# Performance work log

Hardware: AMD Instinct MI355X
Metric: run time of the kernel (lower is better)

The kernel has to match this reference:

```python
import jax, jax.numpy as jnp
import numpy as np

H = 256   # node_hidden_dim == edge_hidden_dim

def _ln(x, g, b):
    m = x.mean(-1, keepdims=True)
    v = ((x - m) ** 2).mean(-1, keepdims=True)
    return (x - m) / jnp.sqrt(v + 1e-5) * g + b

def _slnn(x, W, b, g, beta):
    # Linear -> LayerNorm -> ReLU (SingleLayerNN)
    return jax.nn.relu(_ln(x @ W.T + b, g, beta))

def _gru_mean(x, Wih, Whh, bih, bhh):
    # x: [E, T, Din]; torch GRU gate order (r, z, n); returns mean over time of outputs [E, H]
    h0 = jnp.zeros((x.shape[0], Whh.shape[1]), x.dtype)
    def step(h, xt):
        gi = xt @ Wih.T + bih
        gh = h @ Whh.T + bhh
        ir, iz, inn = jnp.split(gi, 3, axis=-1)
        hr, hz, hn = jnp.split(gh, 3, axis=-1)
        r = jax.nn.sigmoid(ir + hr)
        z = jax.nn.sigmoid(iz + hz)
        n = jnp.tanh(inn + r * hn)
        h_new = (1.0 - z) * n + z * h
        return h_new, h_new
    _, ys = jax.lax.scan(step, h0, jnp.swapaxes(x, 0, 1))  # [T, E, H]
    return ys.mean(axis=0)

def setup_inputs() -> dict:
    key = jax.random.key(0)
    ks = iter(jax.random.split(key, 64))
    rn = lambda shape, s=1.0: (jax.random.normal(next(ks), shape, jnp.float32) * s)
    ru = lambda shape: jax.random.uniform(next(ks), shape, jnp.float32)
    ri = lambda shape, hi: jax.random.randint(next(ks), shape, 0, hi, jnp.int32)
    N0, N1, N2, E0, E1, T = 40000, 10000, 2000, 100000, 20000, 8
    Dn, De, FC, C = 128, 64, 512, 16
    inp = {
        'node_features': rn((N0, Dn)),
        'edge_features_0': rn((E0, T, De)),
        'edge_features_1': rn((E1, T, H)),
        'history_0': rn((N0, H)),
        'history_1': rn((N1, H)),
        'agg_history_1': rn((N2, H)),
        'subg_norm_1': ru((N1, 1)),
        'subg_norm_2': ru((N2, 1)),
        'norm_2': ru((N2, 1)),
        'src0': ri((E0,), N0), 'dst0': ri((E0,), N1),
        'src1': ri((E1,), N1), 'dst1': ri((E1,), N2),
        'self_nid0': ri((N1,), N0), 'self_nid1': ri((N2,), N1),
        # parameters
        'gru0_Wih': rn((3 * H, De), 0.05), 'gru0_Whh': rn((3 * H, H), 0.05),
        'gru0_bih': rn((3 * H,), 0.05), 'gru0_bhh': rn((3 * H,), 0.05),
        'gru1_Wih': rn((3 * H, H), 0.05), 'gru1_Whh': rn((3 * H, H), 0.05),
        'gru1_bih': rn((3 * H,), 0.05), 'gru1_bhh': rn((3 * H,), 0.05),
        'phi0_W': rn((H, Dn + H), 0.05), 'phi0_b': rn((H,), 0.05),
        'phi0_g': jnp.ones((H,)), 'phi0_beta': jnp.zeros((H,)),
        'phi1_W': rn((H, 2 * H), 0.05), 'phi1_b': rn((H,), 0.05),
        'phi1_g': jnp.ones((H,)), 'phi1_beta': jnp.zeros((H,)),
        'nu0_W': rn((H, 2 * H), 0.05), 'nu0_b': rn((H,), 0.05),
        'nu0_g': jnp.ones((H,)), 'nu0_beta': jnp.zeros((H,)),
        'nu1_W': rn((H, 2 * H), 0.05), 'nu1_b': rn((H,), 0.05),
        'nu1_g': jnp.ones((H,)), 'nu1_beta': jnp.zeros((H,)),
        'fc1_W': rn((FC, H), 0.05), 'fc1_b': rn((FC,), 0.05),
        'fc2_W': rn((C, FC), 0.05), 'fc2_b': rn((C,), 0.05),
    }
    return inp

def reference(node_features, edge_features_0, edge_features_1, history_0, history_1,
              agg_history_1, subg_norm_1, subg_norm_2, norm_2,
              gru0_Wih, gru0_Whh, gru0_bih, gru0_bhh,
              gru1_Wih, gru1_Whh, gru1_bih, gru1_bhh,
              phi0_W, phi0_b, phi0_g, phi0_beta,
              phi1_W, phi1_b, phi1_g, phi1_beta,
              nu0_W, nu0_b, nu0_g, nu0_beta,
              nu1_W, nu1_b, nu1_g, nu1_beta,
              fc1_W, fc1_b, fc2_W, fc2_b,
              src0, dst0, src1, dst1, self_nid0, self_nid1):
    N1, N2 = self_nid0.shape[0], self_nid1.shape[0]
    # ---- layer 0 ----
    self_h0 = _slnn(jnp.concatenate([jnp.zeros((N1, H), node_features.dtype),
                                     node_features[self_nid0]], 1),
                    phi0_W, phi0_b, phi0_g, phi0_beta)                       # [N1, H]
    edge_emb0 = _gru_mean(edge_features_0, gru0_Wih, gru0_Whh, gru0_bih, gru0_bhh)  # [E0, H]
    nb0 = _slnn(jnp.concatenate([node_features[src0], edge_emb0], 1),
                phi0_W, phi0_b, phi0_g, phi0_beta)
    msg0 = jax.nn.relu(nb0 - history_0[src0])
    delta_nb0 = jax.ops.segment_sum(msg0, dst0, num_segments=N1)             # scatter-sum
    new_h0 = (delta_nb0 - self_h0) * subg_norm_1
    h1 = _slnn(jnp.concatenate([new_h0, self_h0], 1), nu0_W, nu0_b, nu0_g, nu0_beta)  # [N1, H]
    # ---- layer 1 ----
    self_h1 = _slnn(jnp.concatenate([jnp.zeros((N2, H), h1.dtype), h1[self_nid1]], 1),
                    phi1_W, phi1_b, phi1_g, phi1_beta)                       # [N2, H]
    self_delta_h1 = self_h1 - history_1[self_nid1]
    edge_emb1 = _gru_mean(edge_features_1, gru1_Wih, gru1_Whh, gru1_bih, gru1_bhh)  # [E1, H]
    nb1 = _slnn(jnp.concatenate([h1[src1], edge_emb1], 1),
                phi1_W, phi1_b, phi1_g, phi1_beta)
    msg1 = jax.nn.relu(nb1 - history_1[src1])
    delta_nb1 = jax.ops.segment_sum(msg1, dst1, num_segments=N2)
    new_h1 = (delta_nb1 - self_delta_h1) * subg_norm_2 + agg_history_1 * norm_2
    h2 = _slnn(jnp.concatenate([new_h1, self_h1], 1), nu1_W, nu1_b, nu1_g, nu1_beta)  # [N2, H]
    # ---- readout (no activation between fc1 and fc2, as in source) ----
    logit = (h2 @ fc1_W.T + fc1_b) @ fc2_W.T + fc2_b
    return logit
```

## Files before the change

### kernel.cpp

```cpp
#include <hip/hip_runtime.h>

typedef unsigned short u16;
typedef __attribute__((ext_vector_type(4))) float f32x4;
typedef __attribute__((ext_vector_type(8))) short bf16x8;
#define MFMA16(a,b,c) __builtin_amdgcn_mfma_f32_16x16x32_bf16((a),(b),(c),0,0,0)

__device__ __forceinline__ u16 f2bf(float f){
  unsigned int u = __float_as_uint(f);
  u += 0x7FFFu + ((u >> 16) & 1u);
  return (u16)(u >> 16);
}
__device__ __forceinline__ float bf2f(u16 h){
  return __uint_as_float(((unsigned int)h) << 16);
}
__device__ __forceinline__ float sigmoid_f(float x){
  x = fminf(fmaxf(x, -30.f), 30.f);
  return __fdividef(1.f, 1.f + __expf(-x));
}
__device__ __forceinline__ float tanh_f(float x){
  x = fminf(fmaxf(x, -15.f), 15.f);
  float e = __expf(-2.f * x);
  return __fdividef(1.f - e, 1.f + e);
}

__global__ void cvt_bf16_kernel(const float* __restrict__ in, u16* __restrict__ out, int n){
  int i = blockIdx.x * 256 + threadIdx.x;
  int stride = gridDim.x * 256;
  for (; i < n; i += stride) out[i] = f2bf(in[i]);
}

template<int R>
__device__ __forceinline__ void ln_stats_rows(const float* __restrict__ O,
                                              float* __restrict__ mean_s,
                                              float* __restrict__ rstd_s){
  const int tid  = threadIdx.x;
  const int wave = tid >> 6, lane = tid & 63;
  constexpr int RW = R / 4;
  #pragma unroll
  for (int rr = 0; rr < RW; rr++){
    const int r = wave * RW + rr;
    float s = 0.f, q = 0.f;
    #pragma unroll
    for (int i = lane; i < 256; i += 64){ float v = O[r*256 + i]; s += v; q += v*v; }
    #pragma unroll
    for (int off = 32; off; off >>= 1){ s += __shfl_down(s, off); q += __shfl_down(q, off); }
    if (lane == 0){
      float m   = s * (1.f/256.f);
      float var = q * (1.f/256.f) - m*m;
      mean_s[r] = m;
      rstd_s[r] = rsqrtf(fmaxf(var, 0.f) + 1e-5f);
    }
  }
}

template<int DIN, int NFD>
__global__ __launch_bounds__(256, 2)
void gru_mfma_kernel(int E,
    const float* __restrict__ x,
    const float* __restrict__ nodef,
    const int*   __restrict__ src,
    const int*   __restrict__ dst,
    const float* __restrict__ hist,
    const u16*   __restrict__ Wih,
    const u16*   __restrict__ Whh,
    const float* __restrict__ bih,
    const float* __restrict__ bhh,
    const u16*   __restrict__ phiW,
    const float* __restrict__ phib,
    const float* __restrict__ phig,
    const float* __restrict__ phibeta,
    float* __restrict__ delta)
{
  constexpr int HP  = 264;
  constexpr int XW  = (DIN > NFD) ? DIN : NFD;
  constexpr int XLP = XW + 8;
  constexpr int KP  = NFD + 256;

  __shared__ u16  hb[2 * 32 * HP];
  __shared__ u16  xl[32 * XLP];
  __shared__ float sums_s[4 * 32], sqs_s[4 * 32];
  __shared__ float mean_s[32], rstd_s[32];
  __shared__ int   srcs_s[32], dsts_s[32];

  const int tid  = threadIdx.x;
  const int wave = tid >> 6, lane = tid & 63;
  const int quad = lane >> 4, ln15 = lane & 15;
  const int cbase = wave * 64;
  const int e0   = blockIdx.x * 32;

  if (tid < 32){
    int e = e0 + tid;
    int ec = (e < E) ? e : (E - 1);
    srcs_s[tid] = src[ec];
    dsts_s[tid] = dst[ec];
  }

  int cnt[4];
  float brc[4], bzc[4], bnic[4], bnhc[4], pb[4], gg[4], gb[4];
  #pragma unroll
  for (int nt = 0; nt < 4; nt++){
    int c = cbase + nt*16 + ln15;
    cnt[nt]  = c;
    brc[nt]  = bih[c]       + bhh[c];
    bzc[nt]  = bih[256 + c] + bhh[256 + c];
    bnic[nt] = bih[512 + c];
    bnhc[nt] = bhh[512 + c];
    pb[nt]   = phib[c];
    gg[nt]   = phig[c];
    gb[nt]   = phibeta[c];
  }

  const int aoff = ln15 * HP  + quad * 8;
  const int xoff = ln15 * XLP + quad * 8;
  const int qoff = quad * 8;

  float hs[2][4][4];
  #pragma unroll
  for (int mt = 0; mt < 2; mt++)
    #pragma unroll
    for (int nt = 0; nt < 4; nt++)
      #pragma unroll
      for (int q = 0; q < 4; q++) hs[mt][nt][q] = 0.f;

  const f32x4 zero4 = {0.f, 0.f, 0.f, 0.f};

  for (int t = 0; t < 8; t++){
    __syncthreads();
    {
      constexpr int R4 = DIN / 4;
      for (int i = tid; i < 32 * R4; i += 256){
        int e  = i / R4;
        int k4 = (i - e * R4) * 4;
        int ge = (e0 + e < E) ? (e0 + e) : (E - 1);
        const float4 v = *(const float4*)(x + (size_t)ge * (8 * DIN) + (size_t)t * DIN + k4);
        ushort4 u;
        u.x = f2bf(v.x); u.y = f2bf(v.y); u.z = f2bf(v.z); u.w = f2bf(v.w);
        *(ushort4*)(xl + e * XLP + k4) = u;
      }
    }
    __syncthreads();

    const u16* rd = hb + ((t & 1) ^ 1) * (32 * HP);
    u16*       wr = hb + (t & 1) * (32 * HP);

    #pragma unroll 1
    for (int half = 0; half < 2; half++){
      f32x4 aR[2][2], aZ[2][2], aNI[2][2], aNH[2][2];
      #pragma unroll
      for (int mt = 0; mt < 2; mt++)
        #pragma unroll
        for (int j = 0; j < 2; j++){
          aR[mt][j] = zero4; aZ[mt][j] = zero4; aNI[mt][j] = zero4; aNH[mt][j] = zero4;
        }

      if (t > 0){
        #pragma unroll
        for (int kt = 0; kt < 8; kt++){
          bf16x8 a0 = *(const bf16x8*)(rd + aoff + kt * 32);
          bf16x8 a1 = *(const bf16x8*)(rd + aoff + 16 * HP + kt * 32);
          #pragma unroll
          for (int j = 0; j < 2; j++){
            const int nt = half * 2 + j;
            const u16* bp = Whh + (size_t)cnt[nt] * 256 + kt * 32 + qoff;
            bf16x8 br = *(const bf16x8*)(bp);
            bf16x8 bz = *(const bf16x8*)(bp + 256 * 256);
            bf16x8 bn = *(const bf16x8*)(bp + 512 * 256);
            aR[0][j]  = MFMA16(a0, br, aR[0][j]);  aR[1][j]  = MFMA16(a1, br, aR[1][j]);
            aZ[0][j]  = MFMA16(a0, bz, aZ[0][j]);  aZ[1][j]  = MFMA16(a1, bz, aZ[1][j]);
            aNH[0][j] = MFMA16(a0, bn, aNH[0][j]); aNH[1][j] = MFMA16(a1, bn, aNH[1][j]);
          }
        }
      }
      #pragma unroll
      for (int kt = 0; kt < DIN / 32; kt++){
        bf16x8 a0 = *(const bf16x8*)(xl + xoff + kt * 32);
        bf16x8 a1 = *(const bf16x8*)(xl + xoff + 16 * XLP + kt * 32);
        #pragma unroll
        for (int j = 0; j < 2; j++){
          const int nt = half * 2 + j;
          const u16* bp = Wih + (size_t)cnt[nt] * DIN + kt * 32 + qoff;
          bf16x8 br = *(const bf16x8*)(bp);
          bf16x8 bz = *(const bf16x8*)(bp + 256 * DIN);
          bf16x8 bn = *(const bf16x8*)(bp + 512 * DIN);
          aR[0][j]  = MFMA16(a0, br, aR[0][j]);  aR[1][j]  = MFMA16(a1, br, aR[1][j]);
          aZ[0][j]  = MFMA16(a0, bz, aZ[0][j]);  aZ[1][j]  = MFMA16(a1, bz, aZ[1][j]);
          aNI[0][j] = MFMA16(a0, bn, aNI[0][j]); aNI[1][j] = MFMA16(a1, bn, aNI[1][j]);
        }
      }
      #pragma unroll
      for (int mt = 0; mt < 2; mt++)
        #pragma unroll
        for (int j = 0; j < 2; j++){
          const int nt = half * 2 + j;
          const int c  = cnt[nt];
          #pragma unroll
          for (int q = 0; q < 4; q++){
            const int e = mt * 16 + quad * 4 + q;
            float r = sigmoid_f(aR[mt][j][q] + brc[nt]);
            float z = sigmoid_f(aZ[mt][j][q] + bzc[nt]);
            float n = tanh_f(aNI[mt][j][q] + bnic[nt] + r * (aNH[mt][j][q] + bnhc[nt]));
            float hold = (t > 0) ? bf2f(rd[e * HP + c]) : 0.f;
            float hnew = (1.f - z) * n + z * hold;
            hs[mt][nt][q] += hnew;
            if (t < 7) wr[e * HP + c] = f2bf(hnew);
          }
        }
    }
  }

  __syncthreads();
  {
    u16* eb = hb;
    #pragma unroll
    for (int mt = 0; mt < 2; mt++)
      #pragma unroll
      for (int nt = 0; nt < 4; nt++)
        #pragma unroll
        for (int q = 0; q < 4; q++){
          const int e = mt * 16 + quad * 4 + q;
          eb[e * HP + cnt[nt]] = f2bf(hs[mt][nt][q] * 0.125f);
        }
    constexpr int R4 = NFD / 4;
    for (int i = tid; i < 32 * R4; i += 256){
      int e  = i / R4;
      int k4 = (i - e * R4) * 4;
      const float4 v = *(const float4*)(nodef + (size_t)srcs_s[e] * NFD + k4);
      ushort4 u;
      u.x = f2bf(v.x); u.y = f2bf(v.y); u.z = f2bf(v.z); u.w = f2bf(v.w);
      *(ushort4*)(xl + e * XLP + k4) = u;
    }
  }
  __syncthreads();

  f32x4 P[2][4];
  #pragma unroll
  for (int mt = 0; mt < 2; mt++)
    #pragma unroll
    for (int nt = 0; nt < 4; nt++) P[mt][nt] = zero4;

  #pragma unroll
  for (int kt = 0; kt < NFD / 32; kt++){
    bf16x8 a0 = *(const bf16x8*)(xl + xoff + kt * 32);
    bf16x8 a1 = *(const bf16x8*)(xl + xoff + 16 * XLP + kt * 32);
    #pragma unroll
    for (int nt = 0; nt < 4; nt++){
      const u16* bp = phiW + (size_t)cnt[nt] * KP + kt * 32 + qoff;
      bf16x8 b = *(const bf16x8*)(bp);
      P[0][nt] = MFMA16(a0, b, P[0][nt]);
      P[1][nt] = MFMA16(a1, b, P[1][nt]);
    }
  }
  #pragma unroll
  for (int kt = 0; kt < 8; kt++){
    bf16x8 a0 = *(const bf16x8*)(hb + aoff + kt * 32);
    bf16x8 a1 = *(const bf16x8*)(hb + aoff + 16 * HP + kt * 32);
    #pragma unroll
    for (int nt = 0; nt < 4; nt++){
      const u16* bp = phiW + (size_t)cnt[nt] * KP + NFD + kt * 32 + qoff;
      bf16x8 b = *(const bf16x8*)(bp);
      P[0][nt] = MFMA16(a0, b, P[0][nt]);
      P[1][nt] = MFMA16(a1, b, P[1][nt]);
    }
  }

  float sl[2][4], sq[2][4];
  #pragma unroll
  for (int mt = 0; mt < 2; mt++)
    #pragma unroll
    for (int q = 0; q < 4; q++){ sl[mt][q] = 0.f; sq[mt][q] = 0.f; }
  #pragma unroll
  for (int mt = 0; mt < 2; mt++)
    #pragma unroll
    for (int nt = 0; nt < 4; nt++)
      #pragma unroll
      for (int q = 0; q < 4; q++){
        float v = P[mt][nt][q] + pb[nt];
        P[mt][nt][q] = v;
        sl[mt][q] += v;
        sq[mt][q] += v * v;
      }
  #pragma unroll
  for (int off = 1; off < 16; off <<= 1){
    #pragma unroll
    for (int mt = 0; mt < 2; mt++)
      #pragma unroll
      for (int q = 0; q < 4; q++){
        sl[mt][q] += __shfl_xor(sl[mt][q], off);
        sq[mt][q] += __shfl_xor(sq[mt][q], off);
      }
  }
  if (ln15 == 0){
    #pragma unroll
    for (int mt = 0; mt < 2; mt++)
      #pragma unroll
      for (int q = 0; q < 4; q++){
        int row = mt * 16 + quad * 4 + q;
        sums_s[wave * 32 + row] = sl[mt][q];
        sqs_s[wave * 32 + row]  = sq[mt][q];
      }
  }
  __syncthreads();
  if (tid < 32){
    float m = 0.f, qq = 0.f;
    #pragma unroll
    for (int w = 0; w < 4; w++){ m += sums_s[w * 32 + tid]; qq += sqs_s[w * 32 + tid]; }
    m  *= (1.f / 256.f);
    qq *= (1.f / 256.f);
    mean_s[tid] = m;
    rstd_s[tid] = rsqrtf(fmaxf(qq - m * m, 0.f) + 1e-5f);
  }
  __syncthreads();

  #pragma unroll
  for (int mt = 0; mt < 2; mt++)
    #pragma unroll
    for (int nt = 0; nt < 4; nt++){
      const int c = cnt[nt];
      #pragma unroll
      for (int q = 0; q < 4; q++){
        const int e  = mt * 16 + quad * 4 + q;
        const int ge = e0 + e;
        float y = (P[mt][nt][q] - mean_s[e]) * rstd_s[e] * gg[nt] + gb[nt];
        y = fmaxf(y, 0.f);
        float mv = y - hist[(size_t)srcs_s[e] * 256 + c];
        if (ge < E && mv > 0.f)
          atomicAdd(delta + (size_t)dsts_s[e] * 256 + c, mv);
      }
    }
}

template<int K, int WS>
__global__ __launch_bounds__(256)
void self_slnn_kernel(int N,
    const float* __restrict__ feat,
    const int*   __restrict__ nid,
    const float* __restrict__ W,
    const float* __restrict__ b,
    const float* __restrict__ g,
    const float* __restrict__ beta,
    const float* __restrict__ hist,
    float* __restrict__ out,
    float* __restrict__ out2)
{
  constexpr int R = 8;
  __shared__ float X[R*K];
  __shared__ float O[R*256];
  __shared__ float mean_s[R], rstd_s[R];
  __shared__ int   nids[R];
  const int tid = threadIdx.x;
  const int n0  = blockIdx.x * R;
  if (tid < R) nids[tid] = (n0 + tid < N) ? nid[n0 + tid] : 0;
  __syncthreads();
  for (int i = tid; i < R*K; i += 256){
    int r = i / K, k = i - r*K;
    X[i] = feat[(size_t)nids[r]*K + k];
  }
  __syncthreads();
  const int c = tid;
  const float* Wc = W + (size_t)c*WS + (WS - K);
  float acc[R];
  const float bc0 = b[c];
  #pragma unroll
  for (int r = 0; r < R; r++) acc[r] = bc0;
  #pragma unroll 1
  for (int k = 0; k < K; k += 4){
    float4 w = *(const float4*)(Wc + k);
    #pragma unroll
    for (int r = 0; r < R; r++){
      float4 xv = *(const float4*)(X + r*K + k);
      acc[r] += w.x*xv.x + w.y*xv.y + w.z*xv.z + w.w*xv.w;
    }
  }
  #pragma unroll
  for (int r = 0; r < R; r++) O[r*256 + c] = acc[r];
  __syncthreads();
  ln_stats_rows<R>(O, mean_s, rstd_s);
  __syncthreads();
  const float gc = g[c], bc = beta[c];
  #pragma unroll
  for (int r = 0; r < R; r++){
    int n = n0 + r;
    if (n < N){
      float y = fmaxf((acc[r] - mean_s[r]) * rstd_s[r] * gc + bc, 0.f);
      out[(size_t)n*256 + c] = y;
      if (out2) out2[(size_t)n*256 + c] = y - hist[(size_t)nids[r]*256 + c];
    }
  }
}

__global__ __launch_bounds__(256)
void compose_slnn_kernel(int N,
    const float* __restrict__ delta,
    const float* __restrict__ selfA,
    const float* __restrict__ selfB,
    const float* __restrict__ subg,
    const float* __restrict__ agg,
    const float* __restrict__ normv,
    const float* __restrict__ W,
    const float* __restrict__ b,
    const float* __restrict__ g,
    const float* __restrict__ beta,
    float* __restrict__ out)
{
  constexpr int R = 8;
  __shared__ float X[R*512];
  __shared__ float O[R*256];
  __shared__ float mean_s[R], rstd_s[R];
  const int tid = threadIdx.x;
  const int n0  = blockIdx.x * R;
  for (int i = tid; i < R*512; i += 256){
    int r = i >> 9, k = i & 511;
    int n = n0 + r;
    float v = 0.f;
    if (n < N){
      if (k < 256){
        v = (delta[(size_t)n*256 + k] - selfA[(size_t)n*256 + k]) * subg[n];
        if (agg) v += agg[(size_t)n*256 + k] * normv[n];
      } else {
        v = selfB[(size_t)n*256 + (k - 256)];
      }
    }
    X[i] = v;
  }
  __syncthreads();
  const int c = tid;
  const float* Wc = W + (size_t)c*512;
  float acc[R];
  const float bc0 = b[c];
  #pragma unroll
  for (int r = 0; r < R; r++) acc[r] = bc0;
  #pragma unroll 1
  for (int k = 0; k < 512; k += 4){
    float4 w = *(const float4*)(Wc + k);
    #pragma unroll
    for (int r = 0; r < R; r++){
      float4 xv = *(const float4*)(X + r*512 + k);
      acc[r] += w.x*xv.x + w.y*xv.y + w.z*xv.z + w.w*xv.w;
    }
  }
  #pragma unroll
  for (int r = 0; r < R; r++) O[r*256 + c] = acc[r];
  __syncthreads();
  ln_stats_rows<R>(O, mean_s, rstd_s);
  __syncthreads();
  const float gc = g[c], bc = beta[c];
  #pragma unroll
  for (int r = 0; r < R; r++){
    int n = n0 + r;
    if (n < N)
      out[(size_t)n*256 + c] = fmaxf((acc[r] - mean_s[r]) * rstd_s[r] * gc + bc, 0.f);
  }
}

__global__ __launch_bounds__(256)
void readout_kernel(int N,
    const float* __restrict__ h2,
    const float* __restrict__ W1,
    const float* __restrict__ b1,
    const float* __restrict__ W2,
    const float* __restrict__ b2,
    float* __restrict__ out)
{
  constexpr int R = 8;
  __shared__ float X[R*256];
  __shared__ float T[R*512];
  const int tid = threadIdx.x;
  const int n0  = blockIdx.x * R;
  for (int i = tid; i < R*256; i += 256){
    int r = i >> 8, k = i & 255;
    int n = n0 + r;
    X[i] = (n < N) ? h2[(size_t)n*256 + k] : 0.f;
  }
  __syncthreads();
  const int c = tid;
  const float* Wa = W1 + (size_t)c*256;
  const float* Wb = W1 + (size_t)(c+256)*256;
  float acca[R], accb[R];
  const float ba = b1[c], bb = b1[c+256];
  #pragma unroll
  for (int r = 0; r < R; r++){ acca[r] = ba; accb[r] = bb; }
  #pragma unroll 1
  for (int k = 0; k < 256; k += 4){
    float4 wa = *(const float4*)(Wa + k);
    float4 wb = *(const float4*)(Wb + k);
    #pragma unroll
    for (int r = 0; r < R; r++){
      float4 xv = *(const float4*)(X + r*256 + k);
      acca[r] += wa.x*xv.x + wa.y*xv.y + wa.z*xv.z + wa.w*xv.w;
      accb[r] += wb.x*xv.x + wb.y*xv.y + wb.z*xv.z + wb.w*xv.w;
    }
  }
  #pragma unroll
  for (int r = 0; r < R; r++){ T[r*512 + c] = acca[r]; T[r*512 + 256 + c] = accb[r]; }
  __syncthreads();
  if (tid < R*16){
    int r = tid >> 4, o = tid & 15;
    int n = n0 + r;
    if (n < N){
      float s = b2[o];
      const float* w  = W2 + (size_t)o*512;
      const float* tr = T + r*512;
      #pragma unroll 4
      for (int k = 0; k < 512; k++) s += tr[k]*w[k];
      out[(size_t)n*16 + o] = s;
    }
  }
}

extern "C" void kernel_launch(void* const* d_in, const int* in_sizes, int n_in,
                              void* d_out, int out_size, void* d_ws, size_t ws_size,
                              hipStream_t stream) {
  const float* nf     = (const float*)d_in[0];
  const float* x0     = (const float*)d_in[1];
  const float* x1     = (const float*)d_in[2];
  const float* hist0  = (const float*)d_in[3];
  const float* hist1  = (const float*)d_in[4];
  const float* aggh1  = (const float*)d_in[5];
  const float* subg1  = (const float*)d_in[6];
  const float* subg2  = (const float*)d_in[7];
  const float* norm2  = (const float*)d_in[8];
  const int*   src0   = (const int*)d_in[9];
  const int*   dst0   = (const int*)d_in[10];
  const int*   src1   = (const int*)d_in[11];
  const int*   dst1   = (const int*)d_in[12];
  const int*   nid0   = (const int*)d_in[13];
  const int*   nid1   = (const int*)d_in[14];
  const float* g0Wih  = (const float*)d_in[15];
  const float* g0Whh  = (const float*)d_in[16];
  const float* g0bih  = (const float*)d_in[17];
  const float* g0bhh  = (const float*)d_in[18];
  const float* g1Wih  = (const float*)d_in[19];
  const float* g1Whh  = (const float*)d_in[20];
  const float* g1bih  = (const float*)d_in[21];
  const float* g1bhh  = (const float*)d_in[22];
  const float* phi0W  = (const float*)d_in[23];
  const float* phi0b  = (const float*)d_in[24];
  const float* phi0g  = (const float*)d_in[25];
  const float* phi0be = (const float*)d_in[26];
  const float* phi1W  = (const float*)d_in[27];
  const float* phi1b  = (const float*)d_in[28];
  const float* phi1g  = (const float*)d_in[29];
  const float* phi1be = (const float*)d_in[30];
  const float* nu0W   = (const float*)d_in[31];
  const float* nu0b   = (const float*)d_in[32];
  const float* nu0g   = (const float*)d_in[33];
  const float* nu0be  = (const float*)d_in[34];
  const float* nu1W   = (const float*)d_in[35];
  const float* nu1b   = (const float*)d_in[36];
  const float* nu1g   = (const float*)d_in[37];
  const float* nu1be  = (const float*)d_in[38];
  const float* fc1W   = (const float*)d_in[39];
  const float* fc1b   = (const float*)d_in[40];
  const float* fc2W   = (const float*)d_in[41];
  const float* fc2b   = (const float*)d_in[42];

  const int E0 = in_sizes[9];
  const int E1 = in_sizes[11];
  const int N1 = in_sizes[13];
  const int N2 = in_sizes[14];

  float* ws     = (float*)d_ws;
  float* delta0 = ws;
  float* selfh0 = delta0 + (size_t)N1*256;
  float* h1p    = selfh0 + (size_t)N1*256;
  float* delta1 = h1p    + (size_t)N1*256;
  float* selfh1 = delta1 + (size_t)N2*256;
  float* selfd1 = selfh1 + (size_t)N2*256;
  float* h2p    = selfd1 + (size_t)N2*256;

  u16* wbf       = (u16*)(h2p + (size_t)N2*256);
  u16* g0Wih_bf  = wbf;
  u16* g0Whh_bf  = g0Wih_bf + 768*64;
  u16* phi0W_bf  = g0Whh_bf + 768*256;
  u16* g1Wih_bf  = phi0W_bf + 256*384;
  u16* g1Whh_bf  = g1Wih_bf + 768*256;
  u16* phi1W_bf  = g1Whh_bf + 768*256;

  hipMemsetAsync(delta0, 0, (size_t)N1*256*sizeof(float), stream);
  hipMemsetAsync(delta1, 0, (size_t)N2*256*sizeof(float), stream);

  cvt_bf16_kernel<<<192, 256, 0, stream>>>(g0Wih, g0Wih_bf, 768*64);
  cvt_bf16_kernel<<<768, 256, 0, stream>>>(g0Whh, g0Whh_bf, 768*256);
  cvt_bf16_kernel<<<384, 256, 0, stream>>>(phi0W, phi0W_bf, 256*384);
  cvt_bf16_kernel<<<768, 256, 0, stream>>>(g1Wih, g1Wih_bf, 768*256);
  cvt_bf16_kernel<<<768, 256, 0, stream>>>(g1Whh, g1Whh_bf, 768*256);
  cvt_bf16_kernel<<<512, 256, 0, stream>>>(phi1W, phi1W_bf, 256*512);

  const int gN1 = (N1 + 7) / 8;
  const int gN2 = (N2 + 7) / 8;

  self_slnn_kernel<128, 384><<<gN1, 256, 0, stream>>>(
      N1, nf, nid0, phi0W, phi0b, phi0g, phi0be, nullptr, selfh0, nullptr);

  gru_mfma_kernel<64, 128><<<(E0 + 31) / 32, 256, 0, stream>>>(
      E0, x0, nf, src0, dst0, hist0,
      g0Wih_bf, g0Whh_bf, g0bih, g0bhh,
      phi0W_bf, phi0b, phi0g, phi0be, delta0);

  compose_slnn_kernel<<<gN1, 256, 0, stream>>>(
      N1, delta0, selfh0, selfh0, subg1, nullptr, nullptr,
      nu0W, nu0b, nu0g, nu0be, h1p);

  self_slnn_kernel<256, 512><<<gN2, 256, 0, stream>>>(
      N2, h1p, nid1, phi1W, phi1b, phi1g, phi1be, hist1, selfh1, selfd1);

  gru_mfma_kernel<256, 256><<<(E1 + 31) / 32, 256, 0, stream>>>(
      E1, x1, h1p, src1, dst1, hist1,
      g1Wih_bf, g1Whh_bf, g1bih, g1bhh,
      phi1W_bf, phi1b, phi1g, phi1be, delta1);

  compose_slnn_kernel<<<gN2, 256, 0, stream>>>(
      N2, delta1, selfd1, selfh1, subg2, aggh1, norm2,
      nu1W, nu1b, nu1g, nu1be, h2p);

  readout_kernel<<<gN2, 256, 0, stream>>>(
      N2, h2p, fc1W, fc1b, fc2W, fc2b, (float*)d_out);

  (void)n_in; (void)out_size; (void)ws_size;
}
```

Before: 3.261 ms.

## Retile GRU kernel to 64-edge blocks with weight reuse and prefetched inputs

```diff
diff --git a/kernel.cpp b/kernel.cpp
--- a/kernel.cpp
+++ b/kernel.cpp
@@ -4,6 +4,8 @@
 typedef __attribute__((ext_vector_type(4))) float f32x4;
 typedef __attribute__((ext_vector_type(8))) short bf16x8;
 #define MFMA16(a,b,c) __builtin_amdgcn_mfma_f32_16x16x32_bf16((a),(b),(c),0,0,0)
+
+template<int N> struct ic { static constexpr int v = N; };
 
 __device__ __forceinline__ u16 f2bf(float f){
   unsigned int u = __float_as_uint(f);
@@ -54,7 +56,7 @@
 }
 
 template<int DIN, int NFD>
-__global__ __launch_bounds__(256, 2)
+__global__ __launch_bounds__(512, 2)
 void gru_mfma_kernel(int E,
     const float* __restrict__ x,
     const float* __restrict__ nodef,
@@ -72,35 +74,35 @@
     float* __restrict__ delta)
 {
   constexpr int HP  = 264;
-  constexpr int XW  = (DIN > NFD) ? DIN : NFD;
-  constexpr int XLP = XW + 8;
+  constexpr int XP  = DIN + 8;
+  constexpr int NP  = NFD + 8;
   constexpr int KP  = NFD + 256;
-
-  __shared__ u16  hb[2 * 32 * HP];
-  __shared__ u16  xl[32 * XLP];
-  __shared__ float sums_s[4 * 32], sqs_s[4 * 32];
-  __shared__ float mean_s[32], rstd_s[32];
-  __shared__ int   srcs_s[32], dsts_s[32];
+  constexpr int NF4 = DIN / 32;
+
+  __shared__ u16  hb[2 * 64 * HP];
+  __shared__ u16  xb[2 * 64 * XP];
+  __shared__ float sums_s[8 * 64], sqs_s[8 * 64];
+  __shared__ float mean_s[64], rstd_s[64];
+  __shared__ int   srcs_s[64], dsts_s[64];
 
   const int tid  = threadIdx.x;
   const int wave = tid >> 6, lane = tid & 63;
   const int quad = lane >> 4, ln15 = lane & 15;
-  const int cbase = wave * 64;
-  const int e0   = blockIdx.x * 32;
-
-  if (tid < 32){
-    int e = e0 + tid;
+  const int cbase = wave * 32;
+  const int e0   = blockIdx.x * 64;
+
+  if (tid < 64){
+    int e  = e0 + tid;
     int ec = (e < E) ? e : (E - 1);
     srcs_s[tid] = src[ec];
     dsts_s[tid] = dst[ec];
   }
 
-  int cnt[4];
-  float brc[4], bzc[4], bnic[4], bnhc[4], pb[4], gg[4], gb[4];
-  #pragma unroll
-  for (int nt = 0; nt < 4; nt++){
-    int c = cbase + nt*16 + ln15;
-    cnt[nt]  = c;
+  int cn[2]; float brc[2], bzc[2], bnic[2], bnhc[2], pb[2], gg[2], gb[2];
+  #pragma unroll
+  for (int nt = 0; nt < 2; nt++){
+    int c   = cbase + nt * 16 + ln15;
+    cn[nt]  = c;
     brc[nt]  = bih[c]       + bhh[c];
     bzc[nt]  = bih[256 + c] + bhh[256 + c];
     bnic[nt] = bih[512 + c];
@@ -110,200 +112,219 @@
     gb[nt]   = phibeta[c];
   }
 
-  const int aoff = ln15 * HP  + quad * 8;
-  const int xoff = ln15 * XLP + quad * 8;
-  const int qoff = quad * 8;
+  #pragma unroll
+  for (int j = 0; j < NF4; j++){
+    int i4 = tid + j * 512;
+    int e  = i4 / (DIN / 4);
+    int k4 = (i4 % (DIN / 4)) * 4;
+    int ge = (e0 + e < E) ? (e0 + e) : (E - 1);
+    float4 v = *(const float4*)(x + (size_t)ge * (8 * DIN) + k4);
+    ushort4 u;
+    u.x = f2bf(v.x); u.y = f2bf(v.y); u.z = f2bf(v.z); u.w = f2bf(v.w);
+    *(ushort4*)(xb + e * XP + k4) = u;
+  }
+  __syncthreads();
 
   float hs[2][4][4];
   #pragma unroll
-  for (int mt = 0; mt < 2; mt++)
-    #pragma unroll
-    for (int nt = 0; nt < 4; nt++)
-      #pragma unroll
-      for (int q = 0; q < 4; q++) hs[mt][nt][q] = 0.f;
+  for (int nt = 0; nt < 2; nt++)
+    #pragma unroll
+    for (int mt = 0; mt < 4; mt++)
+      #pragma unroll
+      for (int q = 0; q < 4; q++) hs[nt][mt][q] = 0.f;
 
   const f32x4 zero4 = {0.f, 0.f, 0.f, 0.f};
 
+  #pragma unroll 1
   for (int t = 0; t < 8; t++){
-    __syncthreads();
-    {
-      constexpr int R4 = DIN / 4;
-      for (int i = tid; i < 32 * R4; i += 256){
-        int e  = i / R4;
-        int k4 = (i - e * R4) * 4;
+    const u16* rd = hb + ((t & 1) ^ 1) * (64 * HP);
+    u16*       wr = hb + (t & 1) * (64 * HP);
+    const u16* xr = xb + (t & 1) * (64 * XP);
+
+    float4 xpre[NF4];
+    if (t < 7){
+      #pragma unroll
+      for (int j = 0; j < NF4; j++){
+        int i4 = tid + j * 512;
+        int e  = i4 / (DIN / 4);
+        int k4 = (i4 % (DIN / 4)) * 4;
         int ge = (e0 + e < E) ? (e0 + e) : (E - 1);
-        const float4 v = *(const float4*)(x + (size_t)ge * (8 * DIN) + (size_t)t * DIN + k4);
-        ushort4 u;
-        u.x = f2bf(v.x); u.y = f2bf(v.y); u.z = f2bf(v.z); u.w = f2bf(v.w);
-        *(ushort4*)(xl + e * XLP + k4) = u;
-      }
-    }
-    __syncthreads();
-
-    const u16* rd = hb + ((t & 1) ^ 1) * (32 * HP);
-    u16*       wr = hb + (t & 1) * (32 * HP);
-
-    #pragma unroll 1
-    for (int half = 0; half < 2; half++){
-      f32x4 aR[2][2], aZ[2][2], aNI[2][2], aNH[2][2];
-      #pragma unroll
-      for (int mt = 0; mt < 2; mt++)
-        #pragma unroll
-        for (int j = 0; j < 2; j++){
-          aR[mt][j] = zero4; aZ[mt][j] = zero4; aNI[mt][j] = zero4; aNH[mt][j] = zero4;
-        }
-
+        xpre[j] = *(const float4*)(x + (size_t)ge * (8 * DIN) + (size_t)(t + 1) * DIN + k4);
+      }
+    }
+
+    auto phase = [&](auto ntc){
+      constexpr int NT = decltype(ntc)::v;
+      const int c = cn[NT];
+      f32x4 aR[4], aZ[4], aNI[4], aNH[4];
+      #pragma unroll
+      for (int mt = 0; mt < 4; mt++){
+        aR[mt] = zero4; aZ[mt] = zero4; aNI[mt] = zero4; aNH[mt] = zero4;
+      }
       if (t > 0){
         #pragma unroll
         for (int kt = 0; kt < 8; kt++){
-          bf16x8 a0 = *(const bf16x8*)(rd + aoff + kt * 32);
-          bf16x8 a1 = *(const bf16x8*)(rd + aoff + 16 * HP + kt * 32);
+          bf16x8 a[4];
           #pragma unroll
-          for (int j = 0; j < 2; j++){
-            const int nt = half * 2 + j;
-            const u16* bp = Whh + (size_t)cnt[nt] * 256 + kt * 32 + qoff;
-            bf16x8 br = *(const bf16x8*)(bp);
-            bf16x8 bz = *(const bf16x8*)(bp + 256 * 256);
-            bf16x8 bn = *(const bf16x8*)(bp + 512 * 256);
-            aR[0][j]  = MFMA16(a0, br, aR[0][j]);  aR[1][j]  = MFMA16(a1, br, aR[1][j]);
-            aZ[0][j]  = MFMA16(a0, bz, aZ[0][j]);  aZ[1][j]  = MFMA16(a1, bz, aZ[1][j]);
-            aNH[0][j] = MFMA16(a0, bn, aNH[0][j]); aNH[1][j] = MFMA16(a1, bn, aNH[1][j]);
+          for (int mt = 0; mt < 4; mt++)
+            a[mt] = *(const bf16x8*)(rd + (mt*16 + ln15) * HP + kt * 32 + quad * 8);
+          const u16* bp = Whh + (size_t)c * 256 + kt * 32 + quad * 8;
+          bf16x8 br = *(const bf16x8*)(bp);
+          bf16x8 bz = *(const bf16x8*)(bp + 256 * 256);
+          bf16x8 bn = *(const bf16x8*)(bp + 512 * 256);
+          #pragma unroll
+          for (int mt = 0; mt < 4; mt++){
+            aR[mt]  = MFMA16(a[mt], br, aR[mt]);
+            aZ[mt]  = MFMA16(a[mt], bz, aZ[mt]);
+            aNH[mt] = MFMA16(a[mt], bn, aNH[mt]);
           }
         }
       }
       #pragma unroll
       for (int kt = 0; kt < DIN / 32; kt++){
-        bf16x8 a0 = *(const bf16x8*)(xl + xoff + kt * 32);
-        bf16x8 a1 = *(const bf16x8*)(xl + xoff + 16 * XLP + kt * 32);
+        bf16x8 a[4];
         #pragma unroll
-        for (int j = 0; j < 2; j++){
-          const int nt = half * 2 + j;
-          const u16* bp = Wih + (size_t)cnt[nt] * DIN + kt * 32 + qoff;
-          bf16x8 br = *(const bf16x8*)(bp);
-          bf16x8 bz = *(const bf16x8*)(bp + 256 * DIN);
-          bf16x8 bn = *(const bf16x8*)(bp + 512 * DIN);
-          aR[0][j]  = MFMA16(a0, br, aR[0][j]);  aR[1][j]  = MFMA16(a1, br, aR[1][j]);
-          aZ[0][j]  = MFMA16(a0, bz, aZ[0][j]);  aZ[1][j]  = MFMA16(a1, bz, aZ[1][j]);
-          aNI[0][j] = MFMA16(a0, bn, aNI[0][j]); aNI[1][j] = MFMA16(a1, bn, aNI[1][j]);
+        for (int mt = 0; mt < 4; mt++)
+          a[mt] = *(const bf16x8*)(xr + (mt*16 + ln15) * XP + kt * 32 + quad * 8);
+        const u16* bp = Wih + (size_t)c * DIN + kt * 32 + quad * 8;
+        bf16x8 br = *(const bf16x8*)(bp);
+        bf16x8 bz = *(const bf16x8*)(bp + 256 * DIN);
+        bf16x8 bn = *(const bf16x8*)(bp + 512 * DIN);
+        #pragma unroll
+        for (int mt = 0; mt < 4; mt++){
+          aR[mt]  = MFMA16(a[mt], br, aR[mt]);
+          aZ[mt]  = MFMA16(a[mt], bz, aZ[mt]);
+          aNI[mt] = MFMA16(a[mt], bn, aNI[mt]);
         }
       }
       #pragma unroll
-      for (int mt = 0; mt < 2; mt++)
-        #pragma unroll
-        for (int j = 0; j < 2; j++){
-          const int nt = half * 2 + j;
-          const int c  = cnt[nt];
-          #pragma unroll
-          for (int q = 0; q < 4; q++){
-            const int e = mt * 16 + quad * 4 + q;
-            float r = sigmoid_f(aR[mt][j][q] + brc[nt]);
-            float z = sigmoid_f(aZ[mt][j][q] + bzc[nt]);
-            float n = tanh_f(aNI[mt][j][q] + bnic[nt] + r * (aNH[mt][j][q] + bnhc[nt]));
-            float hold = (t > 0) ? bf2f(rd[e * HP + c]) : 0.f;
-            float hnew = (1.f - z) * n + z * hold;
-            hs[mt][nt][q] += hnew;
-            if (t < 7) wr[e * HP + c] = f2bf(hnew);
-          }
-        }
-    }
-  }
-
-  __syncthreads();
-  {
-    u16* eb = hb;
-    #pragma unroll
-    for (int mt = 0; mt < 2; mt++)
-      #pragma unroll
-      for (int nt = 0; nt < 4; nt++)
+      for (int mt = 0; mt < 4; mt++){
         #pragma unroll
         for (int q = 0; q < 4; q++){
           const int e = mt * 16 + quad * 4 + q;
-          eb[e * HP + cnt[nt]] = f2bf(hs[mt][nt][q] * 0.125f);
+          float r = sigmoid_f(aR[mt][q] + brc[NT]);
+          float z = sigmoid_f(aZ[mt][q] + bzc[NT]);
+          float n = tanh_f(aNI[mt][q] + bnic[NT] + r * (aNH[mt][q] + bnhc[NT]));
+          float hold = (t > 0) ? bf2f(rd[e * HP + c]) : 0.f;
+          float hnew = (1.f - z) * n + z * hold;
+          hs[NT][mt][q] += hnew;
+          if (t < 7) wr[e * HP + c] = f2bf(hnew);
+        }
+      }
+    };
+    phase(ic<0>());
+    phase(ic<1>());
+
+    if (t < 7){
+      u16* xw = xb + ((t + 1) & 1) * (64 * XP);
+      #pragma unroll
+      for (int j = 0; j < NF4; j++){
+        int i4 = tid + j * 512;
+        int e  = i4 / (DIN / 4);
+        int k4 = (i4 % (DIN / 4)) * 4;
+        ushort4 u;
+        u.x = f2bf(xpre[j].x); u.y = f2bf(xpre[j].y);
+        u.z = f2bf(xpre[j].z); u.w = f2bf(xpre[j].w);
+        *(ushort4*)(xw + e * XP + k4) = u;
+      }
+    }
+    __syncthreads();
+  }
+
+  {
+    u16* eb = hb;
+    #pragma unroll
+    for (int nt = 0; nt < 2; nt++)
+      #pragma unroll
+      for (int mt = 0; mt < 4; mt++)
+        #pragma unroll
+        for (int q = 0; q < 4; q++){
+          const int e = mt * 16 + quad * 4 + q;
+          eb[e * HP + cn[nt]] = f2bf(hs[nt][mt][q] * 0.125f);
         }
     constexpr int R4 = NFD / 4;
-    for (int i = tid; i < 32 * R4; i += 256){
+    for (int i = tid; i < 64 * R4; i += 512){
       int e  = i / R4;
       int k4 = (i - e * R4) * 4;
       const float4 v = *(const float4*)(nodef + (size_t)srcs_s[e] * NFD + k4);
       ushort4 u;
       u.x = f2bf(v.x); u.y = f2bf(v.y); u.z = f2bf(v.z); u.w = f2bf(v.w);
-      *(ushort4*)(xl + e * XLP + k4) = u;
+      *(ushort4*)(xb + e * NP + k4) = u;
     }
   }
   __syncthreads();
 
   f32x4 P[2][4];
   #pragma unroll
-  for (int mt = 0; mt < 2; mt++)
-    #pragma unroll
-    for (int nt = 0; nt < 4; nt++) P[mt][nt] = zero4;
+  for (int nt = 0; nt < 2; nt++)
+    #pragma unroll
+    for (int mt = 0; mt < 4; mt++) P[nt][mt] = zero4;
 
   #pragma unroll
   for (int kt = 0; kt < NFD / 32; kt++){
-    bf16x8 a0 = *(const bf16x8*)(xl + xoff + kt * 32);
-    bf16x8 a1 = *(const bf16x8*)(xl + xoff + 16 * XLP + kt * 32);
-    #pragma unroll
-    for (int nt = 0; nt < 4; nt++){
-      const u16* bp = phiW + (size_t)cnt[nt] * KP + kt * 32 + qoff;
+    bf16x8 a[4];
+    #pragma unroll
+    for (int mt = 0; mt < 4; mt++)
+      a[mt] = *(const bf16x8*)(xb + (mt*16 + ln15) * NP + kt * 32 + quad * 8);
+    #pragma unroll
+    for (int nt = 0; nt < 2; nt++){
+      const u16* bp = phiW + (size_t)cn[nt] * KP + kt * 32 + quad * 8;
       bf16x8 b = *(const bf16x8*)(bp);
-      P[0][nt] = MFMA16(a0, b, P[0][nt]);
-      P[1][nt] = MFMA16(a1, b, P[1][nt]);
+      #pragma unroll
+      for (int mt = 0; mt < 4; mt++) P[nt][mt] = MFMA16(a[mt], b, P[nt][mt]);
     }
   }
   #pragma unroll
   for (int kt = 0; kt < 8; kt++){
-    bf16x8 a0 = *(const bf16x8*)(hb + aoff + kt * 32);
-    bf16x8 a1 = *(const bf16x8*)(hb + aoff + 16 * HP + kt * 32);
-    #pragma unroll
-    for (int nt = 0; nt < 4; nt++){
-      const u16* bp = phiW + (size_t)cnt[nt] * KP + NFD + kt * 32 + qoff;
+    bf16x8 a[4];
+    #pragma unroll
+    for (int mt = 0; mt < 4; mt++)
+      a[mt] = *(const bf16x8*)(hb + (mt*16 + ln15) * HP + kt * 32 + quad * 8);
+    #pragma unroll
+    for (int nt = 0; nt < 2; nt++){
+      const u16* bp = phiW + (size_t)cn[nt] * KP + NFD + kt * 32 + quad * 8;
       bf16x8 b = *(const bf16x8*)(bp);
-      P[0][nt] = MFMA16(a0, b, P[0][nt]);
-      P[1][nt] = MFMA16(a1, b, P[1][nt]);
-    }
-  }
-
-  float sl[2][4], sq[2][4];
-  #pragma unroll
-  for (int mt = 0; mt < 2; mt++)
-    #pragma unroll
-    for (int q = 0; q < 4; q++){ sl[mt][q] = 0.f; sq[mt][q] = 0.f; }
-  #pragma unroll
-  for (int mt = 0; mt < 2; mt++)
-    #pragma unroll
-    for (int nt = 0; nt < 4; nt++)
+      #pragma unroll
+      for (int mt = 0; mt < 4; mt++) P[nt][mt] = MFMA16(a[mt], b, P[nt][mt]);
+    }
+  }
+
+  float sl[4][4], sq_[4][4];
+  #pragma unroll
+  for (int mt = 0; mt < 4; mt++)
+    #pragma unroll
+    for (int q = 0; q < 4; q++){
+      float v0 = P[0][mt][q] + pb[0];
+      float v1 = P[1][mt][q] + pb[1];
+      P[0][mt][q] = v0; P[1][mt][q] = v1;
+      sl[mt][q]  = v0 + v1;
+      sq_[mt][q] = v0 * v0 + v1 * v1;
+    }
+  #pragma unroll
+  for (int off = 1; off < 16; off <<= 1){
+    #pragma unroll
+    for (int mt = 0; mt < 4; mt++)
       #pragma unroll
       for (int q = 0; q < 4; q++){
-        float v = P[mt][nt][q] + pb[nt];
-        P[mt][nt][q] = v;
-        sl[mt][q] += v;
-        sq[mt][q] += v * v;
-      }
-  #pragma unroll
-  for (int off = 1; off < 16; off <<= 1){
-    #pragma unroll
-    for (int mt = 0; mt < 2; mt++)
-      #pragma unroll
-      for (int q = 0; q < 4; q++){
-        sl[mt][q] += __shfl_xor(sl[mt][q], off);
-        sq[mt][q] += __shfl_xor(sq[mt][q], off);
+        sl[mt][q]  += __shfl_xor(sl[mt][q], off);
+        sq_[mt][q] += __shfl_xor(sq_[mt][q], off);
       }
   }
   if (ln15 == 0){
     #pragma unroll
-    for (int mt = 0; mt < 2; mt++)
+    for (int mt = 0; mt < 4; mt++)
       #pragma unroll
       for (int q = 0; q < 4; q++){
         int row = mt * 16 + quad * 4 + q;
-        sums_s[wave * 32 + row] = sl[mt][q];
-        sqs_s[wave * 32 + row]  = sq[mt][q];
-      }
-  }
-  __syncthreads();
-  if (tid < 32){
+        sums_s[wave * 64 + row] = sl[mt][q];
+        sqs_s[wave * 64 + row]  = sq_[mt][q];
+      }
+  }
+  __syncthreads();
+  if (tid < 64){
     float m = 0.f, qq = 0.f;
     #pragma unroll
-    for (int w = 0; w < 4; w++){ m += sums_s[w * 32 + tid]; qq += sqs_s[w * 32 + tid]; }
+    for (int w = 0; w < 8; w++){ m += sums_s[w * 64 + tid]; qq += sqs_s[w * 64 + tid]; }
     m  *= (1.f / 256.f);
     qq *= (1.f / 256.f);
     mean_s[tid] = m;
@@ -312,21 +333,21 @@
   __syncthreads();
 
   #pragma unroll
-  for (int mt = 0; mt < 2; mt++)
-    #pragma unroll
-    for (int nt = 0; nt < 4; nt++){
-      const int c = cnt[nt];
+  for (int nt = 0; nt < 2; nt++){
+    const int c = cn[nt];
+    #pragma unroll
+    for (int mt = 0; mt < 4; mt++)
       #pragma unroll
       for (int q = 0; q < 4; q++){
         const int e  = mt * 16 + quad * 4 + q;
         const int ge = e0 + e;
-        float y = (P[mt][nt][q] - mean_s[e]) * rstd_s[e] * gg[nt] + gb[nt];
+        float y = (P[nt][mt][q] - mean_s[e]) * rstd_s[e] * gg[nt] + gb[nt];
         y = fmaxf(y, 0.f);
         float mv = y - hist[(size_t)srcs_s[e] * 256 + c];
         if (ge < E && mv > 0.f)
           atomicAdd(delta + (size_t)dsts_s[e] * 256 + c, mv);
       }
-    }
+  }
 }
 
 template<int K, int WS>
@@ -592,7 +613,7 @@
   self_slnn_kernel<128, 384><<<gN1, 256, 0, stream>>>(
       N1, nf, nid0, phi0W, phi0b, phi0g, phi0be, nullptr, selfh0, nullptr);
 
-  gru_mfma_kernel<64, 128><<<(E0 + 31) / 32, 256, 0, stream>>>(
+  gru_mfma_kernel<64, 128><<<(E0 + 63) / 64, 512, 0, stream>>>(
       E0, x0, nf, src0, dst0, hist0,
       g0Wih_bf, g0Whh_bf, g0bih, g0bhh,
       phi0W_bf, phi0b, phi0g, phi0be, delta0);
@@ -604,7 +625,7 @@
   self_slnn_kernel<256, 512><<<gN2, 256, 0, stream>>>(
       N2, h1p, nid1, phi1W, phi1b, phi1g, phi1be, hist1, selfh1, selfd1);
 
-  gru_mfma_kernel<256, 256><<<(E1 + 31) / 32, 256, 0, stream>>>(
+  gru_mfma_kernel<256, 256><<<(E1 + 63) / 64, 512, 0, stream>>>(
       E1, x1, h1p, src1, dst1, hist1,
       g1Wih_bf, g1Whh_bf, g1bih, g1bhh,
       phi1W_bf, phi1b, phi1g, phi1be, delta1);
```

Measured after the change: 2.812 ms. 1.16x faster.
